# Kernel tuning notes

Hardware: AMD Instinct MI355X
Metric: run time of the kernel (lower is better)

The kernel has to match this reference:

```python
import math
import jax, jax.numpy as jnp
import numpy as np

SCALE = math.sqrt(128.0)  # NOTE: original code MULTIPLIES by sqrt(128)
DROPOUT_P = 0.1


def setup_inputs() -> dict:
    key = jax.random.key(0)
    kq, kk, kv = jax.random.split(key, 3)
    B, Q, V, H = 4, 4096, 4096, 128
    return {
        "query": jax.random.normal(kq, (B, Q, H), dtype=jnp.float32),
        "key": jax.random.normal(kk, (B, V, H), dtype=jnp.float32),
        "value": jax.random.normal(kv, (B, V, H), dtype=jnp.float32),
    }


def reference(query, key, value):
    # qk: [B, Q, V]
    qk = jnp.einsum("bqh,bvh->bqv", query, key)
    scaled_qk = qk * SCALE
    softmax_qk = jax.nn.softmax(scaled_qk, axis=-1)
    # inverted dropout with a fixed RNG key (deterministic reference)
    dk = jax.random.key(42)
    keep = jax.random.bernoulli(dk, 1.0 - DROPOUT_P, softmax_qk.shape)
    dropout_qk = jnp.where(keep, softmax_qk / (1.0 - DROPOUT_P), 0.0)
    # output: [B, Q, H]
    return jnp.einsum("bqv,bvh->bqh", dropout_qk, value)
```

## Files before the change

### kernel.cpp

```cpp
#include <hip/hip_runtime.h>
#include <stdint.h>

#define NBATCH 4
#define NQ 4096
#define NV 4096
#define HD 128

#define SCL2E ((float)(11.31370849898476 * 1.4426950408889634))

#define KEEP_THRESH 3865470464u

#define SKIP_MARGIN 27.0f
#define DROP_MARGIN 20.0f

#define TILE_USH 24576
#define WS_NEEDED ((size_t)NBATCH * 64 * TILE_USH * 2)

#define PSTR 72
#define VLSTR 142

#define KSTR 144
#define VSTR 76

typedef __attribute__((ext_vector_type(8))) short short8;
typedef __attribute__((ext_vector_type(4))) float floatx4;
typedef unsigned int uint;
typedef unsigned short ushort;

__device__ __forceinline__ ushort bf16rne(float f) {
    uint u = __float_as_uint(f);
    u = (u + 0x7fffu + ((u >> 16) & 1u)) >> 16;
    return (ushort)u;
}
__device__ __forceinline__ float bf2f(ushort h) {
    return __uint_as_float(((uint)h) << 16);
}

template <int CTRL>
__device__ __forceinline__ float dppmov(float x) {
    return __int_as_float(__builtin_amdgcn_update_dpp(
        0, __float_as_int(x), CTRL, 0xF, 0xF, true));
}
__device__ __forceinline__ float row_max16(float x) {
    x = fmaxf(x, dppmov<0xB1>(x));
    x = fmaxf(x, dppmov<0x4E>(x));
    x = fmaxf(x, dppmov<0x141>(x));
    x = fmaxf(x, dppmov<0x140>(x));
    return x;
}
__device__ __forceinline__ float row_sum16(float x) {
    x += dppmov<0xB1>(x);
    x += dppmov<0x4E>(x);
    x += dppmov<0x141>(x);
    x += dppmov<0x140>(x);
    return x;
}

__device__ __forceinline__ uint rotl(uint x, int r) { return (x << r) | (x >> (32 - r)); }

__device__ __forceinline__ uint threefry_bits(uint j) {
    uint x0 = 0u;
    uint x1 = j;
    const uint k0 = 0u, k1 = 42u, k2 = 0u ^ 42u ^ 0x1BD11BDAu;
    x0 += k0; x1 += k1;
#define TFR4(a,b,c,d) \
    x0 += x1; x1 = rotl(x1, a); x1 ^= x0; \
    x0 += x1; x1 = rotl(x1, b); x1 ^= x0; \
    x0 += x1; x1 = rotl(x1, c); x1 ^= x0; \
    x0 += x1; x1 = rotl(x1, d); x1 ^= x0;
    TFR4(13, 15, 26, 6)
    x0 += k1; x1 += k2 + 1u;
    TFR4(17, 29, 16, 24)
    x0 += k2; x1 += k0 + 2u;
    TFR4(13, 15, 26, 6)
    x0 += k0; x1 += k1 + 3u;
    TFR4(17, 29, 16, 24)
    x0 += k1; x1 += k2 + 4u;
    TFR4(13, 15, 26, 6)
    x0 += k2; x1 += k0 + 5u;
#undef TFR4
    return x0 ^ x1;
}

__global__ __launch_bounds__(256)
void prepass(const float* __restrict__ Kg, const float* __restrict__ Vg,
             ushort* __restrict__ W) {
    __shared__ ushort vls[64 * VLSTR];
    const int rec  = blockIdx.x >> 1;
    const int half = blockIdx.x & 1;
    const int bb = rec >> 6;
    const int t  = rec & 63;
    const int v0 = t * 64;
    const size_t kvbase = (size_t)bb * NV * HD;
    ushort* dst = W + ((size_t)bb * 64 + t) * TILE_USH;
    const int tid = threadIdx.x;

    if (half == 0) {
        ushort* dkh = dst;
        ushort* dkl = dst + 8192;
#pragma unroll
        for (int i = 0; i < 4; ++i) {
            int lc = i * 256 + tid;
            int v = lc >> 4, c = lc & 15;
            const float* src = Kg + kvbase + (size_t)(v0 + v) * HD + c * 8;
            float x[8];
            *(float4*)&x[0] = *(const float4*)src;
            *(float4*)&x[4] = *(const float4*)(src + 4);
            uint H[4], L[4];
#pragma unroll
            for (int k = 0; k < 4; ++k) {
                ushort h0 = bf16rne(x[2 * k]),     h1 = bf16rne(x[2 * k + 1]);
                ushort l0 = bf16rne(x[2 * k] - bf2f(h0));
                ushort l1 = bf16rne(x[2 * k + 1] - bf2f(h1));
                H[k] = (uint)h0 | ((uint)h1 << 16);
                L[k] = (uint)l0 | ((uint)l1 << 16);
            }
            int pos = (((c >> 2) * 4 + (v >> 4)) * 64 + (c & 3) * 16 + (v & 15)) * 8;
            *(uint4*)&dkh[pos] = *(uint4*)H;
            *(uint4*)&dkl[pos] = *(uint4*)L;
        }
    } else {
        ushort* dvt = dst + 16384;
#pragma unroll
        for (int i = 0; i < 8; ++i) {
            int idx = i * 256 + tid;
            int v = idx >> 5, hq = idx & 31;
            float4 a = *(const float4*)(Vg + kvbase + (size_t)(v0 + v) * HD + hq * 4);
            uint w0 = (uint)bf16rne(a.x) | ((uint)bf16rne(a.y) << 16);
            uint w1 = (uint)bf16rne(a.z) | ((uint)bf16rne(a.w) << 16);
            *(uint*)&vls[v * VLSTR + hq * 4]     = w0;
            *(uint*)&vls[v * VLSTR + hq * 4 + 2] = w1;
        }
        __syncthreads();
#pragma unroll
        for (int i = 0; i < 4; ++i) {
            int lc = i * 256 + tid;
            int h = lc >> 3, c2 = lc & 7;
            uint Wd[4];
#pragma unroll
            for (int m = 0; m < 8; m += 2) {
                ushort a  = vls[(c2 * 8 + m) * VLSTR + h];
                ushort b2 = vls[(c2 * 8 + m + 1) * VLSTR + h];
                Wd[m >> 1] = (uint)a | ((uint)b2 << 16);
            }
            int pos = (((c2 >> 2) * 8 + (h >> 4)) * 64 + (c2 & 3) * 16 + (h & 15)) * 8;
            *(uint4*)&dvt[pos] = *(uint4*)Wd;
        }
    }
}

__global__ __launch_bounds__(256, 2)
void fa_mfma7(const float* __restrict__ Qg, const ushort* __restrict__ Wk,
              float* __restrict__ Og) {
    __shared__ __align__(16) float smemf[12288];
    __shared__ float mlbuf[3][32][2];
    __shared__ float gmx[32];

    const int tid  = threadIdx.x;
    const int wave = tid >> 6;
    const int lane = tid & 63;
    const int r    = lane & 15;
    const int qd   = lane >> 4;
    const int blockRow0 = blockIdx.x * 32;
    const int b = blockRow0 >> 12;
    const ushort* kvw = Wk + (size_t)b * 64 * TILE_USH;
    ushort* pls = (ushort*)smemf + wave * (32 * PSTR);

    if (tid < 32) gmx[tid] = -1e30f;

    short8 qfh[2][4], qfl[2][4];
#pragma unroll
    for (int mr = 0; mr < 2; ++mr) {
        const float* qp = Qg + (size_t)(blockRow0 + mr * 16 + r) * HD + qd * 8;
#pragma unroll
        for (int kc = 0; kc < 4; ++kc) {
            float x[8];
            *(float4*)&x[0] = *(const float4*)(qp + kc * 32);
            *(float4*)&x[4] = *(const float4*)(qp + kc * 32 + 4);
#pragma unroll
            for (int j = 0; j < 8; ++j) {
                float xs = x[j] * SCL2E;
                ushort h = bf16rne(xs);
                qfh[mr][kc][j] = (short)h;
                qfl[mr][kc][j] = (short)bf16rne(xs - bf2f(h));
            }
        }
    }

    floatx4 oacc[2][8];
#pragma unroll
    for (int mr = 0; mr < 2; ++mr)
#pragma unroll
        for (int n = 0; n < 8; ++n) oacc[mr][n] = (floatx4){0.f, 0.f, 0.f, 0.f};
    float m2[2][4], lr[2][4];
#pragma unroll
    for (int mr = 0; mr < 2; ++mr)
#pragma unroll
        for (int g = 0; g < 4; ++g) { m2[mr][g] = -1e30f; lr[mr][g] = 0.f; }

    __syncthreads();

    for (int t = wave; t < 64; t += 4) {
        const ushort* tK = kvw + (size_t)t * TILE_USH;
        const ushort* tV = tK + 16384;
        const int v0 = t * 64;

        floatx4 cf[2][4];
#pragma unroll
        for (int mr = 0; mr < 2; ++mr)
#pragma unroll
            for (int nb = 0; nb < 4; ++nb) cf[mr][nb] = (floatx4){0.f, 0.f, 0.f, 0.f};
#pragma unroll
        for (int kc = 0; kc < 4; ++kc) {
            short8 kh[4], kl[4];
#pragma unroll
            for (int nb = 0; nb < 4; ++nb) {
                int off = ((kc * 4 + nb) * 64 + lane) * 8;
                kh[nb] = *(const short8*)&tK[off];
                kl[nb] = *(const short8*)&tK[8192 + off];
            }
#pragma unroll
            for (int nb = 0; nb < 4; ++nb)
#pragma unroll
                for (int mr = 0; mr < 2; ++mr) {
                    cf[mr][nb] = __builtin_amdgcn_mfma_f32_16x16x32_bf16(qfh[mr][kc], kh[nb], cf[mr][nb], 0, 0, 0);
                    cf[mr][nb] = __builtin_amdgcn_mfma_f32_16x16x32_bf16(qfh[mr][kc], kl[nb], cf[mr][nb], 0, 0, 0);
                    cf[mr][nb] = __builtin_amdgcn_mfma_f32_16x16x32_bf16(qfl[mr][kc], kh[nb], cf[mr][nb], 0, 0, 0);
                }
        }

        bool act[2];
#pragma unroll
        for (int mr = 0; mr < 2; ++mr) {
            float tmx[4], gm[4];
#pragma unroll
            for (int g = 0; g < 4; ++g) {
                float v = fmaxf(fmaxf(cf[mr][0][g], cf[mr][1][g]),
                                fmaxf(cf[mr][2][g], cf[mr][3][g]));
                tmx[g] = row_max16(v);
            }
            bool rowact = false;
#pragma unroll
            for (int g = 0; g < 4; ++g) {
                gm[g] = gmx[mr * 16 + qd * 4 + g];
                rowact |= (tmx[g] > fmaxf(m2[mr][g], gm[g]) - SKIP_MARGIN);
            }
#pragma unroll
            for (int g = 0; g < 4; ++g)
                if (r == 0 && tmx[g] > gm[g]) gmx[mr * 16 + qd * 4 + g] = tmx[g];
            act[mr] = __any(rowact);
            if (!act[mr]) continue;

            float alpha[4];
            bool nm = false;
#pragma unroll
            for (int g = 0; g < 4; ++g) nm |= (tmx[g] > m2[mr][g]);
            if (__any(nm)) {
#pragma unroll
                for (int g = 0; g < 4; ++g) {
                    float mn = fmaxf(m2[mr][g], tmx[g]);
                    alpha[g] = __builtin_amdgcn_exp2f(m2[mr][g] - mn);
                    m2[mr][g] = mn;
                }
#pragma unroll
                for (int n = 0; n < 8; ++n)
#pragma unroll
                    for (int g = 0; g < 4; ++g) oacc[mr][n][g] *= alpha[g];
            } else {
#pragma unroll
                for (int g = 0; g < 4; ++g) alpha[g] = 1.f;
            }

            float p[4][4], thr[4];
#pragma unroll
            for (int g = 0; g < 4; ++g) {
                float s = 0.f;
#pragma unroll
                for (int nb = 0; nb < 4; ++nb) {
                    p[nb][g] = __builtin_amdgcn_exp2f(cf[mr][nb][g] - m2[mr][g]);
                    s += p[nb][g];
                }
                s = row_sum16(s);
                lr[mr][g] = lr[mr][g] * alpha[g] + s;
                thr[g] = fmaxf(gm[g], m2[mr][g]) - DROP_MARGIN;
            }

#pragma unroll
            for (int nb = 0; nb < 4; ++nb) {
#pragma unroll
                for (int g = 0; g < 4; ++g) {
                    if (__any(cf[mr][nb][g] > thr[g])) {
                        uint j = (uint)(blockRow0 + mr * 16 + qd * 4 + g) * (uint)NV
                               + (uint)(v0 + nb * 16 + r);
                        if (threefry_bits(j) >= KEEP_THRESH) p[nb][g] = 0.f;
                    }
                    pls[(mr * 16 + qd * 4 + g) * PSTR + nb * 16 + r] =
                        (ushort)(__float_as_uint(p[nb][g]) >> 16);
                }
            }
        }

        if (act[0] | act[1]) {
            __asm__ volatile("s_waitcnt lgkmcnt(0)" ::: "memory");
#pragma unroll
            for (int mr = 0; mr < 2; ++mr) {
                if (!act[mr]) continue;
#pragma unroll
                for (int kc2 = 0; kc2 < 2; ++kc2) {
                    short8 pa = *(const short8*)&pls[(mr * 16 + r) * PSTR + kc2 * 32 + qd * 8];
#pragma unroll
                    for (int n = 0; n < 8; ++n) {
                        short8 vb = *(const short8*)&tV[((kc2 * 8 + n) * 64 + lane) * 8];
                        oacc[mr][n] = __builtin_amdgcn_mfma_f32_16x16x32_bf16(pa, vb, oacc[mr][n], 0, 0, 0);
                    }
                }
            }
        }
    }

    __syncthreads();
    if (wave >= 1) {
#pragma unroll
        for (int mr = 0; mr < 2; ++mr) {
            if (r == 0) {
#pragma unroll
                for (int g = 0; g < 4; ++g) {
                    mlbuf[wave - 1][mr * 16 + qd * 4 + g][0] = m2[mr][g];
                    mlbuf[wave - 1][mr * 16 + qd * 4 + g][1] = lr[mr][g];
                }
            }
#pragma unroll
            for (int n = 0; n < 8; ++n)
#pragma unroll
                for (int g = 0; g < 4; ++g)
                    smemf[(wave - 1) * 4096 + (mr * 16 + qd * 4 + g) * 128 + n * 16 + r] =
                        oacc[mr][n][g];
        }
    }
    __syncthreads();
    if (wave == 0) {
#pragma unroll
        for (int mr = 0; mr < 2; ++mr) {
            float a0[4], aw[3][4], inv[4];
#pragma unroll
            for (int g = 0; g < 4; ++g) {
                int row = mr * 16 + qd * 4 + g;
                float mn = m2[mr][g];
#pragma unroll
                for (int i = 0; i < 3; ++i) mn = fmaxf(mn, mlbuf[i][row][0]);
                a0[g] = __builtin_amdgcn_exp2f(m2[mr][g] - mn);
                float l = lr[mr][g] * a0[g];
#pragma unroll
                for (int i = 0; i < 3; ++i) {
                    aw[i][g] = __builtin_amdgcn_exp2f(mlbuf[i][row][0] - mn);
                    l += mlbuf[i][row][1] * aw[i][g];
                }
                inv[g] = 1.0f / (0.9f * l);
            }
#pragma unroll
            for (int n = 0; n < 8; ++n)
#pragma unroll
                for (int g = 0; g < 4; ++g) {
                    int row = mr * 16 + qd * 4 + g;
                    float o = oacc[mr][n][g] * a0[g];
#pragma unroll
                    for (int i = 0; i < 3; ++i)
                        o += smemf[i * 4096 + row * 128 + n * 16 + r] * aw[i][g];
                    Og[(size_t)(blockRow0 + row) * HD + n * 16 + r] = o * inv[g];
                }
        }
    }
}

__global__ __launch_bounds__(256)
void fa_mfma(const float* __restrict__ Qg, const float* __restrict__ Kg,
             const float* __restrict__ Vg, float* __restrict__ Og) {
    __shared__ ushort khi[64 * KSTR];
    __shared__ ushort klo[64 * KSTR];
    __shared__ ushort vt[128 * VSTR];
    __shared__ ushort plsf[4][16 * PSTR];

    const int tid  = threadIdx.x;
    const int wave = tid >> 6;
    const int lane = tid & 63;
    const int r    = lane & 15;
    const int qd   = lane >> 4;
    const int blockRow0 = blockIdx.x * 64;
    const int b = blockRow0 >> 12;
    const int waveRow0 = blockRow0 + wave * 16;
    const size_t kvbase = (size_t)b * NV * HD;

    short8 qfh[4], qfl[4];
    {
        const float* qp = Qg + (size_t)(waveRow0 + r) * HD + qd * 8;
#pragma unroll
        for (int kc = 0; kc < 4; ++kc) {
            float x[8];
            *(float4*)&x[0] = *(const float4*)(qp + kc * 32);
            *(float4*)&x[4] = *(const float4*)(qp + kc * 32 + 4);
#pragma unroll
            for (int j = 0; j < 8; ++j) {
                ushort h = bf16rne(x[j]);
                qfh[kc][j] = (short)h;
                qfl[kc][j] = (short)bf16rne(x[j] - bf2f(h));
            }
        }
    }

    floatx4 oacc[8];
#pragma unroll
    for (int n = 0; n < 8; ++n) oacc[n] = (floatx4){0.f, 0.f, 0.f, 0.f};
    float m2[4] = {-INFINITY, -INFINITY, -INFINITY, -INFINITY};
    float lr[4] = {0.f, 0.f, 0.f, 0.f};

    for (int v0 = 0; v0 < NV; v0 += 64) {
        __syncthreads();
#pragma unroll
        for (int i = 0; i < 8; ++i) {
            int f = i * 256 + tid;
            int v = f >> 5;
            int h = (f & 31) * 4;
            float4 kv = *(const float4*)(Kg + kvbase + (size_t)(v0 + v) * HD + h);
            ushort4 hh, ll;
            hh.x = bf16rne(kv.x); ll.x = bf16rne(kv.x - bf2f(hh.x));
            hh.y = bf16rne(kv.y); ll.y = bf16rne(kv.y - bf2f(hh.y));
            hh.z = bf16rne(kv.z); ll.z = bf16rne(kv.z - bf2f(hh.z));
            hh.w = bf16rne(kv.w); ll.w = bf16rne(kv.w - bf2f(hh.w));
            *(ushort4*)&khi[v * KSTR + h] = hh;
            *(ushort4*)&klo[v * KSTR + h] = ll;
        }
        {
            int hp = tid & 63, rp = tid >> 6;
            int h = hp * 2;
            const float* vpb = Vg + kvbase + (size_t)v0 * HD + h;
#pragma unroll
            for (int i = 0; i < 8; ++i) {
                int v = i * 8 + rp * 2;
                float2 a = *(const float2*)(vpb + (size_t)v * HD);
                float2 c = *(const float2*)(vpb + (size_t)(v + 1) * HD);
                uint w0 = (uint)bf16rne(a.x) | ((uint)bf16rne(c.x) << 16);
                uint w1 = (uint)bf16rne(a.y) | ((uint)bf16rne(c.y) << 16);
                *(uint*)&vt[h * VSTR + v]       = w0;
                *(uint*)&vt[(h + 1) * VSTR + v] = w1;
            }
        }
        __syncthreads();

        floatx4 cf[4];
#pragma unroll
        for (int nb = 0; nb < 4; ++nb) cf[nb] = (floatx4){0.f, 0.f, 0.f, 0.f};
#pragma unroll
        for (int kc = 0; kc < 4; ++kc) {
#pragma unroll
            for (int nb = 0; nb < 4; ++nb) {
                int off = (nb * 16 + r) * KSTR + kc * 32 + qd * 8;
                short8 kh = *(const short8*)&khi[off];
                short8 kl = *(const short8*)&klo[off];
                cf[nb] = __builtin_amdgcn_mfma_f32_16x16x32_bf16(qfh[kc], kh, cf[nb], 0, 0, 0);
                cf[nb] = __builtin_amdgcn_mfma_f32_16x16x32_bf16(qfh[kc], kl, cf[nb], 0, 0, 0);
                cf[nb] = __builtin_amdgcn_mfma_f32_16x16x32_bf16(qfl[kc], kh, cf[nb], 0, 0, 0);
            }
        }

        float ts[4][4], p[4][4];
#pragma unroll
        for (int nb = 0; nb < 4; ++nb)
#pragma unroll
            for (int g = 0; g < 4; ++g) ts[nb][g] = cf[nb][g] * SCL2E;

        float tsum[4], alpha[4], lnew[4];
#pragma unroll
        for (int g = 0; g < 4; ++g) {
            float tmx = fmaxf(fmaxf(ts[0][g], ts[1][g]), fmaxf(ts[2][g], ts[3][g]));
#pragma unroll
            for (int off = 1; off < 16; off <<= 1)
                tmx = fmaxf(tmx, __shfl_xor(tmx, off));
            float mn = fmaxf(m2[g], tmx);
            alpha[g] = __builtin_amdgcn_exp2f(m2[g] - mn);
            m2[g] = mn;
        }
#pragma unroll
        for (int g = 0; g < 4; ++g) {
            float s = 0.f;
#pragma unroll
            for (int nb = 0; nb < 4; ++nb) {
                p[nb][g] = __builtin_amdgcn_exp2f(ts[nb][g] - m2[g]);
                s += p[nb][g];
            }
#pragma unroll
            for (int off = 1; off < 16; off <<= 1)
                s += __shfl_xor(s, off);
            tsum[g] = s;
            lnew[g] = lr[g] * alpha[g] + s;
            lr[g] = lnew[g];
        }

        bool rowneed = false;
#pragma unroll
        for (int g = 0; g < 4; ++g) rowneed |= (tsum[g] > 1e-8f * lnew[g]);

        if (__any(rowneed)) {
#pragma unroll
            for (int n = 0; n < 8; ++n)
#pragma unroll
                for (int g = 0; g < 4; ++g) oacc[n][g] *= alpha[g];

#pragma unroll
            for (int nb = 0; nb < 4; ++nb) {
                bool nbneed = false;
#pragma unroll
                for (int g = 0; g < 4; ++g) nbneed |= (p[nb][g] > 1e-8f * lnew[g]);
                if (__any(nbneed)) {
#pragma unroll
                    for (int g = 0; g < 4; ++g) {
                        uint j = (uint)(waveRow0 + qd * 4 + g) * (uint)NV
                               + (uint)(v0 + nb * 16 + r);
                        if (threefry_bits(j) >= KEEP_THRESH) p[nb][g] = 0.f;
                    }
                }
#pragma unroll
                for (int g = 0; g < 4; ++g)
                    plsf[wave][(qd * 4 + g) * PSTR + nb * 16 + r] = bf16rne(p[nb][g]);
            }
            __asm__ volatile("s_waitcnt lgkmcnt(0)" ::: "memory");

#pragma unroll
            for (int kc2 = 0; kc2 < 2; ++kc2) {
                short8 pa = *(const short8*)&plsf[wave][r * PSTR + kc2 * 32 + qd * 8];
#pragma unroll
                for (int n = 0; n < 8; ++n) {
                    int off = (n * 16 + r) * VSTR + kc2 * 32 + qd * 8;
                    ushort4 u0 = *(const ushort4*)&vt[off];
                    ushort4 u1 = *(const ushort4*)&vt[off + 4];
                    short8 vb;
                    vb[0] = (short)u0.x; vb[1] = (short)u0.y; vb[2] = (short)u0.z; vb[3] = (short)u0.w;
                    vb[4] = (short)u1.x; vb[5] = (short)u1.y; vb[6] = (short)u1.z; vb[7] = (short)u1.w;
                    oacc[n] = __builtin_amdgcn_mfma_f32_16x16x32_bf16(pa, vb, oacc[n], 0, 0, 0);
                }
            }
        }
    }

    float inv[4];
#pragma unroll
    for (int g = 0; g < 4; ++g) inv[g] = 1.0f / (0.9f * lr[g]);
#pragma unroll
    for (int n = 0; n < 8; ++n)
#pragma unroll
        for (int g = 0; g < 4; ++g)
            Og[(size_t)(waveRow0 + qd * 4 + g) * HD + n * 16 + r] = oacc[n][g] * inv[g];
}

extern "C" void kernel_launch(void* const* d_in, const int* in_sizes, int n_in,
                              void* d_out, int out_size, void* d_ws, size_t ws_size,
                              hipStream_t stream) {
    (void)in_sizes; (void)n_in; (void)out_size;
    const float* Qg = (const float*)d_in[0];
    const float* Kg = (const float*)d_in[1];
    const float* Vg = (const float*)d_in[2];
    float* Og = (float*)d_out;
    if (ws_size >= WS_NEEDED) {
        ushort* W = (ushort*)d_ws;
        prepass<<<dim3(512), 256, 0, stream>>>(Kg, Vg, W);
        fa_mfma7<<<dim3(NBATCH * NQ / 32), 256, 0, stream>>>(Qg, (const ushort*)W, Og);
    } else {
        fa_mfma<<<dim3(NBATCH * NQ / 64), 256, 0, stream>>>(Qg, Kg, Vg, Og);
    }
}
```

Measured before the change: 197.7 us.

## Software-pipeline QK MFMA with double-buffered K loads and next-tile prefetch

Restructures the per-wave tile loop so the QK^T MFMAs for the next tile are issued before the PV MFMAs of the current tile. K fragments are double-buffered across kc steps, and the first chunk of the following tile is prefetched. The aim is to hide global/LDS load latency and overlap softmax/dropout scalar work with matrix ops. It raises register pressure from the extra K buffers and the early-computed cf, which may reduce occupancy or cause spills.

```diff
diff --git a/kernel.cpp b/kernel.cpp
--- a/kernel.cpp
+++ b/kernel.cpp
@@ -200,34 +200,56 @@
 
     __syncthreads();
 
+    short8 khA[4], klA[4], khB[4], klB[4];
+    floatx4 cf[2][4];
+
+#define LOADK(H, L, t_, kc_)                                              \
+    {                                                                     \
+        const ushort* tKp_ = kvw + (size_t)(t_) * TILE_USH;               \
+        _Pragma("unroll")                                                 \
+        for (int nb_ = 0; nb_ < 4; ++nb_) {                               \
+            const int off_ = (((kc_) * 4 + nb_) * 64 + lane) * 8;         \
+            H[nb_] = *(const short8*)&tKp_[off_];                         \
+            L[nb_] = *(const short8*)&tKp_[8192 + off_];                  \
+        }                                                                 \
+    }
+
+#define QKM(kc_, H, L)                                                    \
+    {                                                                     \
+        _Pragma("unroll")                                                 \
+        for (int nb_ = 0; nb_ < 4; ++nb_) {                               \
+            _Pragma("unroll")                                             \
+            for (int mr_ = 0; mr_ < 2; ++mr_) {                           \
+                cf[mr_][nb_] = __builtin_amdgcn_mfma_f32_16x16x32_bf16(   \
+                    qfh[mr_][kc_], H[nb_], cf[mr_][nb_], 0, 0, 0);        \
+                cf[mr_][nb_] = __builtin_amdgcn_mfma_f32_16x16x32_bf16(   \
+                    qfh[mr_][kc_], L[nb_], cf[mr_][nb_], 0, 0, 0);        \
+                cf[mr_][nb_] = __builtin_amdgcn_mfma_f32_16x16x32_bf16(   \
+                    qfl[mr_][kc_], H[nb_], cf[mr_][nb_], 0, 0, 0);        \
+            }                                                             \
+        }                                                                 \
+    }
+
+#define QKBLOCK(t_, tpf_)                                                 \
+    {                                                                     \
+        _Pragma("unroll")                                                 \
+        for (int mr_ = 0; mr_ < 2; ++mr_) {                               \
+            _Pragma("unroll")                                             \
+            for (int nb_ = 0; nb_ < 4; ++nb_)                             \
+                cf[mr_][nb_] = (floatx4){0.f, 0.f, 0.f, 0.f};             \
+        }                                                                 \
+        LOADK(khB, klB, t_, 1);   QKM(0, khA, klA);                       \
+        LOADK(khA, klA, t_, 2);   QKM(1, khB, klB);                       \
+        LOADK(khB, klB, t_, 3);   QKM(2, khA, klA);                       \
+        LOADK(khA, klA, tpf_, 0); QKM(3, khB, klB);                       \
+    }
+
+    LOADK(khA, klA, wave, 0);
+    QKBLOCK(wave, wave + 4);
+
     for (int t = wave; t < 64; t += 4) {
-        const ushort* tK = kvw + (size_t)t * TILE_USH;
-        const ushort* tV = tK + 16384;
+        const ushort* tV = kvw + (size_t)t * TILE_USH + 16384;
         const int v0 = t * 64;
-
-        floatx4 cf[2][4];
-#pragma unroll
-        for (int mr = 0; mr < 2; ++mr)
-#pragma unroll
-            for (int nb = 0; nb < 4; ++nb) cf[mr][nb] = (floatx4){0.f, 0.f, 0.f, 0.f};
-#pragma unroll
-        for (int kc = 0; kc < 4; ++kc) {
-            short8 kh[4], kl[4];
-#pragma unroll
-            for (int nb = 0; nb < 4; ++nb) {
-                int off = ((kc * 4 + nb) * 64 + lane) * 8;
-                kh[nb] = *(const short8*)&tK[off];
-                kl[nb] = *(const short8*)&tK[8192 + off];
-            }
-#pragma unroll
-            for (int nb = 0; nb < 4; ++nb)
-#pragma unroll
-                for (int mr = 0; mr < 2; ++mr) {
-                    cf[mr][nb] = __builtin_amdgcn_mfma_f32_16x16x32_bf16(qfh[mr][kc], kh[nb], cf[mr][nb], 0, 0, 0);
-                    cf[mr][nb] = __builtin_amdgcn_mfma_f32_16x16x32_bf16(qfh[mr][kc], kl[nb], cf[mr][nb], 0, 0, 0);
-                    cf[mr][nb] = __builtin_amdgcn_mfma_f32_16x16x32_bf16(qfl[mr][kc], kh[nb], cf[mr][nb], 0, 0, 0);
-                }
-        }
 
         bool act[2];
 #pragma unroll
@@ -300,6 +322,12 @@
             }
         }
 
+        if (t + 4 < 64) {
+            const int tn  = t + 4;
+            const int tpp = (t + 8 < 64) ? (t + 8) : tn;
+            QKBLOCK(tn, tpp);
+        }
+
         if (act[0] | act[1]) {
             __asm__ volatile("s_waitcnt lgkmcnt(0)" ::: "memory");
 #pragma unroll
@@ -317,6 +345,9 @@
             }
         }
     }
+#undef QKBLOCK
+#undef QKM
+#undef LOADK
 
     __syncthreads();
     if (wave >= 1) {
```

After: 254.7 us. +28.8%, slower.

## Screen tiles with a cheap hi-only QK product before the split-bf16 correction

Applied to the files above, without the earlier changes.

The QK score is first computed with only the hi*hi bf16 MFMA and used to decide whether a tile can matter. Only when that screen passes are the two correction MFMAs (hi*lo, lo*hi) run and the softmax and PV work done. The skip and drop margins are widened to absorb the error of the coarse estimate. This removes two thirds of the QK MFMAs on tiles that get skipped, at the cost of loading K twice and recomputing the row max on tiles that stay active.

```diff
diff --git a/kernel.cpp b/kernel.cpp
--- a/kernel.cpp
+++ b/kernel.cpp
@@ -10,8 +10,9 @@
 
 #define KEEP_THRESH 3865470464u
 
-#define SKIP_MARGIN 27.0f
-#define DROP_MARGIN 20.0f
+#define EBOUND 10.0f
+#define SCREEN_MARGIN 47.0f
+#define DROP_MARGIN 30.0f
 
 #define TILE_USH 24576
 #define WS_NEEDED ((size_t)NBATCH * 64 * TILE_USH * 2)
@@ -212,27 +213,22 @@
             for (int nb = 0; nb < 4; ++nb) cf[mr][nb] = (floatx4){0.f, 0.f, 0.f, 0.f};
 #pragma unroll
         for (int kc = 0; kc < 4; ++kc) {
-            short8 kh[4], kl[4];
-#pragma unroll
-            for (int nb = 0; nb < 4; ++nb) {
-                int off = ((kc * 4 + nb) * 64 + lane) * 8;
-                kh[nb] = *(const short8*)&tK[off];
-                kl[nb] = *(const short8*)&tK[8192 + off];
-            }
+            short8 kh[4];
 #pragma unroll
             for (int nb = 0; nb < 4; ++nb)
-#pragma unroll
-                for (int mr = 0; mr < 2; ++mr) {
+                kh[nb] = *(const short8*)&tK[((kc * 4 + nb) * 64 + lane) * 8];
+#pragma unroll
+            for (int nb = 0; nb < 4; ++nb)
+#pragma unroll
+                for (int mr = 0; mr < 2; ++mr)
                     cf[mr][nb] = __builtin_amdgcn_mfma_f32_16x16x32_bf16(qfh[mr][kc], kh[nb], cf[mr][nb], 0, 0, 0);
-                    cf[mr][nb] = __builtin_amdgcn_mfma_f32_16x16x32_bf16(qfh[mr][kc], kl[nb], cf[mr][nb], 0, 0, 0);
-                    cf[mr][nb] = __builtin_amdgcn_mfma_f32_16x16x32_bf16(qfl[mr][kc], kh[nb], cf[mr][nb], 0, 0, 0);
-                }
-        }
-
-        bool act[2];
+        }
+
+        bool sact[2];
+        float gm[2][4];
 #pragma unroll
         for (int mr = 0; mr < 2; ++mr) {
-            float tmx[4], gm[4];
+            float tmx[4];
 #pragma unroll
             for (int g = 0; g < 4; ++g) {
                 float v = fmaxf(fmaxf(cf[mr][0][g], cf[mr][1][g]),
@@ -242,69 +238,98 @@
             bool rowact = false;
 #pragma unroll
             for (int g = 0; g < 4; ++g) {
-                gm[g] = gmx[mr * 16 + qd * 4 + g];
-                rowact |= (tmx[g] > fmaxf(m2[mr][g], gm[g]) - SKIP_MARGIN);
+                gm[mr][g] = gmx[mr * 16 + qd * 4 + g];
+                rowact |= (tmx[g] > fmaxf(m2[mr][g], gm[mr][g]) - SCREEN_MARGIN);
             }
 #pragma unroll
             for (int g = 0; g < 4; ++g)
-                if (r == 0 && tmx[g] > gm[g]) gmx[mr * 16 + qd * 4 + g] = tmx[g];
-            act[mr] = __any(rowact);
-            if (!act[mr]) continue;
-
-            float alpha[4];
-            bool nm = false;
-#pragma unroll
-            for (int g = 0; g < 4; ++g) nm |= (tmx[g] > m2[mr][g]);
-            if (__any(nm)) {
+                if (r == 0 && tmx[g] > gm[mr][g]) gmx[mr * 16 + qd * 4 + g] = tmx[g];
+            sact[mr] = __any(rowact);
+        }
+
+        if (sact[0] | sact[1]) {
+#pragma unroll
+            for (int kc = 0; kc < 4; ++kc) {
+                short8 kh[4], kl[4];
+#pragma unroll
+                for (int nb = 0; nb < 4; ++nb) {
+                    int off = ((kc * 4 + nb) * 64 + lane) * 8;
+                    kh[nb] = *(const short8*)&tK[off];
+                    kl[nb] = *(const short8*)&tK[8192 + off];
+                }
+#pragma unroll
+                for (int nb = 0; nb < 4; ++nb)
+#pragma unroll
+                    for (int mr = 0; mr < 2; ++mr)
+                        if (sact[mr]) {
+                            cf[mr][nb] = __builtin_amdgcn_mfma_f32_16x16x32_bf16(qfh[mr][kc], kl[nb], cf[mr][nb], 0, 0, 0);
+                            cf[mr][nb] = __builtin_amdgcn_mfma_f32_16x16x32_bf16(qfl[mr][kc], kh[nb], cf[mr][nb], 0, 0, 0);
+                        }
+            }
+
+#pragma unroll
+            for (int mr = 0; mr < 2; ++mr) {
+                if (!sact[mr]) continue;
+                float ctx[4];
 #pragma unroll
                 for (int g = 0; g < 4; ++g) {
-                    float mn = fmaxf(m2[mr][g], tmx[g]);
-                    alpha[g] = __builtin_amdgcn_exp2f(m2[mr][g] - mn);
-                    m2[mr][g] = mn;
-                }
-#pragma unroll
-                for (int n = 0; n < 8; ++n)
-#pragma unroll
-                    for (int g = 0; g < 4; ++g) oacc[mr][n][g] *= alpha[g];
-            } else {
-#pragma unroll
-                for (int g = 0; g < 4; ++g) alpha[g] = 1.f;
-            }
-
-            float p[4][4], thr[4];
-#pragma unroll
-            for (int g = 0; g < 4; ++g) {
-                float s = 0.f;
+                    float v = fmaxf(fmaxf(cf[mr][0][g], cf[mr][1][g]),
+                                    fmaxf(cf[mr][2][g], cf[mr][3][g]));
+                    ctx[g] = row_max16(v);
+                }
+                float alpha[4];
+                bool nm = false;
+#pragma unroll
+                for (int g = 0; g < 4; ++g) nm |= (ctx[g] > m2[mr][g]);
+                if (__any(nm)) {
+#pragma unroll
+                    for (int g = 0; g < 4; ++g) {
+                        float mn = fmaxf(m2[mr][g], ctx[g]);
+                        alpha[g] = __builtin_amdgcn_exp2f(m2[mr][g] - mn);
+                        m2[mr][g] = mn;
+                    }
+#pragma unroll
+                    for (int n = 0; n < 8; ++n)
+#pragma unroll
+                        for (int g = 0; g < 4; ++g) oacc[mr][n][g] *= alpha[g];
+                } else {
+#pragma unroll
+                    for (int g = 0; g < 4; ++g) alpha[g] = 1.f;
+                }
+
+                float p[4][4], thr[4];
+#pragma unroll
+                for (int g = 0; g < 4; ++g) {
+                    float s = 0.f;
+#pragma unroll
+                    for (int nb = 0; nb < 4; ++nb) {
+                        p[nb][g] = __builtin_amdgcn_exp2f(cf[mr][nb][g] - m2[mr][g]);
+                        s += p[nb][g];
+                    }
+                    s = row_sum16(s);
+                    lr[mr][g] = lr[mr][g] * alpha[g] + s;
+                    thr[g] = fmaxf(gm[mr][g], m2[mr][g]) - DROP_MARGIN;
+                }
+
 #pragma unroll
                 for (int nb = 0; nb < 4; ++nb) {
-                    p[nb][g] = __builtin_amdgcn_exp2f(cf[mr][nb][g] - m2[mr][g]);
-                    s += p[nb][g];
-                }
-                s = row_sum16(s);
-                lr[mr][g] = lr[mr][g] * alpha[g] + s;
-                thr[g] = fmaxf(gm[g], m2[mr][g]) - DROP_MARGIN;
-            }
-
-#pragma unroll
-            for (int nb = 0; nb < 4; ++nb) {
-#pragma unroll
-                for (int g = 0; g < 4; ++g) {
-                    if (__any(cf[mr][nb][g] > thr[g])) {
-                        uint j = (uint)(blockRow0 + mr * 16 + qd * 4 + g) * (uint)NV
-                               + (uint)(v0 + nb * 16 + r);
-                        if (threefry_bits(j) >= KEEP_THRESH) p[nb][g] = 0.f;
+#pragma unroll
+                    for (int g = 0; g < 4; ++g) {
+                        if (__any(cf[mr][nb][g] > thr[g])) {
+                            uint j = (uint)(blockRow0 + mr * 16 + qd * 4 + g) * (uint)NV
+                                   + (uint)(v0 + nb * 16 + r);
+                            if (threefry_bits(j) >= KEEP_THRESH) p[nb][g] = 0.f;
+                        }
+                        pls[(mr * 16 + qd * 4 + g) * PSTR + nb * 16 + r] =
+                            (ushort)(__float_as_uint(p[nb][g]) >> 16);
                     }
-                    pls[(mr * 16 + qd * 4 + g) * PSTR + nb * 16 + r] =
-                        (ushort)(__float_as_uint(p[nb][g]) >> 16);
-                }
-            }
-        }
-
-        if (act[0] | act[1]) {
+                }
+            }
+
             __asm__ volatile("s_waitcnt lgkmcnt(0)" ::: "memory");
 #pragma unroll
             for (int mr = 0; mr < 2; ++mr) {
-                if (!act[mr]) continue;
+                if (!sact[mr]) continue;
 #pragma unroll
                 for (int kc2 = 0; kc2 < 2; ++kc2) {
                     short8 pa = *(const short8*)&pls[(mr * 16 + r) * PSTR + kc2 * 32 + qd * 8];
```

After: 235.2 us. 18.9% more time.
